# Kernel tuning notes

Measured on AMD Instinct MI355X. Metric: run time of the kernel, lower is better.

Reference implementation:

```python
import jax, jax.numpy as jnp
import numpy as np

B, E, T = 8192, 512, 32


def setup_inputs() -> dict:
    key = jax.random.key(0)
    k1, k2, k3, k4, k5, k6 = jax.random.split(key, 6)
    s1 = 1.0 / np.sqrt(E)  # torch nn.Linear default init scale (uniform bound)
    return {
        "g_exp": jax.random.normal(k1, (B, E), dtype=jnp.float32),
        "tissue_vector": jax.random.randint(k2, (B, 1), 0, T, dtype=jnp.int64),
        # per-tissue head params: Linear(E,E) then Linear(E,1)
        "W1": jax.random.uniform(k3, (T, E, E), jnp.float32, -s1, s1),
        "b1": jax.random.uniform(k4, (T, E), jnp.float32, -s1, s1),
        "W2": jax.random.uniform(k5, (T, E), jnp.float32, -s1, s1),
        "b2": jax.random.uniform(k6, (T,), jnp.float32, -s1, s1),
    }


def reference(g_exp, tissue_vector, W1, b1, W2, b2):
    # Each sample b is routed through the MLP head of its tissue id.
    # Vectorized: run every sample through every tissue head, then select.
    # h[b,t,:] = GELU(g_exp[b] @ W1[t] + b1[t])
    h = jax.nn.gelu(jnp.einsum("be,teh->bth", g_exp, W1) + b1[None, :, :],
                    approximate=False)  # exact erf GELU, matches torch nn.GELU
    # y[b,t] = softplus(h[b,t] @ W2[t] + b2[t])   (Softplus since loss_fn='poisson')
    y = jax.nn.softplus(jnp.einsum("bth,th->bt", h, W2) + b2[None, :])
    tid = tissue_vector[:, 0]  # [B], tissue id per sample
    return jnp.take_along_axis(y, tid[:, None], axis=1)  # [B, 1]
```

## Files before the change

kernel.cpp:

```cpp
#include <hip/hip_runtime.h>
#include <hip/hip_bf16.h>
#include <math.h>

#define B_N 8192
#define E_N 512
#define T_N 32
#define BP 520

typedef short bf16x8 __attribute__((ext_vector_type(8)));
typedef float f32x4 __attribute__((ext_vector_type(4)));

#define WS_OFFS   256
#define WS_RANK   512
#define WS_ORDER  33280
#define WS_YACC   66048
#define WS_YACC8  98816
#define WS_REQ    (WS_YACC8 + 8 * B_N * 4)

typedef __attribute__((address_space(1))) const unsigned int gas_u32;
typedef __attribute__((address_space(3))) unsigned int las_u32;

static __device__ __forceinline__ unsigned short f2bf(float f) {
    unsigned int u = __float_as_uint(f);
    unsigned int r = u + 0x7fffu + ((u >> 16) & 1u);
    return (unsigned short)(r >> 16);
}

static __device__ __forceinline__ unsigned int pk2(float a, float b) {
    __hip_bfloat162 h = __float22bfloat162_rn(float2{a, b});
    unsigned int u;
    __builtin_memcpy(&u, &h, 4);
    return u;
}

__global__ __launch_bounds__(512, 1) void k_gemm_mfma(
    const float* __restrict__ g_exp, const float* __restrict__ W1,
    const int* __restrict__ tv, const float* __restrict__ b1,
    const float* __restrict__ W2, float* __restrict__ yacc8) {
    int wi = blockIdx.x;
    int t = wi & 31, nt = wi >> 5;
    int n0 = nt * 64;

    int tid = threadIdx.x;
    int w = tid >> 6, lane = tid & 63;
    int quad = (lane >> 4) & 3, l15 = lane & 15;

    __shared__ __align__(16) unsigned short Bs[64 * BP];
    __shared__ __align__(16) float As[3][128 * 32];
    __shared__ int rows_s[512];
    __shared__ int wsum[8];

    float b1v[4], w2v[4];
#pragma unroll
    for (int ni = 0; ni < 4; ++ni) {
        int n = t * E_N + n0 + ni * 16 + l15;
        b1v[ni] = b1[n];
        w2v[ni] = W2[n];
    }

    int tvals[16];
    const int4* tvp = (const int4*)(tv + tid * 16);
#pragma unroll
    for (int j = 0; j < 4; ++j) ((int4*)tvals)[j] = tvp[j];
    int myc = 0;
#pragma unroll
    for (int j = 0; j < 16; ++j) myc += (tvals[j] == t) ? 1 : 0;
    int inc = myc;
#pragma unroll
    for (int o = 1; o < 64; o <<= 1) {
        int u = __shfl_up(inc, o, 64);
        if (lane >= o) inc += u;
    }
    if (lane == 63) wsum[w] = inc;
    rows_s[tid] = 0;
    __syncthreads();
    int n_t = 0, wbase = 0;
#pragma unroll
    for (int i = 0; i < 8; ++i) {
        int v = wsum[i];
        n_t += v;
        if (i < w) wbase += v;
    }
    int nt_c = n_t > 512 ? 512 : n_t;
    int rk = wbase + inc - myc;
#pragma unroll
    for (int j = 0; j < 16; ++j)
        if (tvals[j] == t) {
            int rr = rk++;
            if (rr < 512) rows_s[rr] = tid * 16 + j;
        }

    const float* Wsrc = W1 + (size_t)t * E_N * E_N + n0;
    unsigned int* Bw = (unsigned int*)Bs;
#pragma unroll
    for (int i = 0; i < 8; ++i) {
        int flat = i * 512 + tid;
        int k2 = flat >> 4, nq = flat & 15;
        float4 va = *(const float4*)(Wsrc + (size_t)(2 * k2) * E_N + nq * 4);
        float4 vb = *(const float4*)(Wsrc + (size_t)(2 * k2 + 1) * E_N + nq * 4);
        Bw[(nq * 4 + 0) * 260 + k2] = pk2(va.x, vb.x);
        Bw[(nq * 4 + 1) * 260 + k2] = pk2(va.y, vb.y);
        Bw[(nq * 4 + 2) * 260 + k2] = pk2(va.z, vb.z);
        Bw[(nq * 4 + 3) * 260 + k2] = pk2(va.w, vb.w);
    }
    __syncthreads();

    int d0 = tid, d1 = tid + 512;
    int ar0 = d0 >> 3, ac0 = (d0 & 7) ^ (ar0 & 7);
    int ar1 = d1 >> 3, ac1 = (d1 & 7) ^ (ar1 & 7);

    int lrow = w * 16 + l15;
    int c0 = (quad * 2) ^ (lrow & 7);
    int c1 = (quad * 2 + 1) ^ (lrow & 7);

    float* slab = yacc8 + (size_t)nt * B_N;

    int MC = (nt_c + 127) >> 7;
    for (int mc = 0; mc < MC; ++mc) {
        const float* pA0 = g_exp + (size_t)rows_s[mc * 128 + ar0] * E_N + ac0 * 4;
        const float* pA1 = g_exp + (size_t)rows_s[mc * 128 + ar1] * E_N + ac1 * 4;

#define ISSUE(kk) do {                                                                      \
        __builtin_amdgcn_global_load_lds((gas_u32*)(pA0 + (kk) * 32),                       \
                                         (las_u32*)&As[(kk) % 3][d0 * 4], 16, 0, 0);        \
        __builtin_amdgcn_global_load_lds((gas_u32*)(pA1 + (kk) * 32),                       \
                                         (las_u32*)&As[(kk) % 3][d1 * 4], 16, 0, 0);        \
    } while (0)

        ISSUE(0);
        ISSUE(1);

        f32x4 acc[4];
#pragma unroll
        for (int ni = 0; ni < 4; ++ni) acc[ni] = (f32x4){0.f, 0.f, 0.f, 0.f};

#define STAGE(it, W) do {                                                                   \
        asm volatile("s_waitcnt vmcnt(%0)" :: "n"(W) : "memory");                           \
        asm volatile("s_barrier" ::: "memory");                                             \
        const float* Ab = &As[(it) % 3][0];                                                 \
        f32x4 lo = *(const f32x4*)(Ab + (lrow * 8 + c0) * 4);                               \
        f32x4 hi = *(const f32x4*)(Ab + (lrow * 8 + c1) * 4);                               \
        unsigned int uu[4] = {pk2(lo[0], lo[1]), pk2(lo[2], lo[3]),                         \
                              pk2(hi[0], hi[1]), pk2(hi[2], hi[3])};                        \
        bf16x8 af;                                                                          \
        __builtin_memcpy(&af, uu, 16);                                                      \
        _Pragma("unroll") for (int ni = 0; ni < 4; ++ni) {                                  \
            bf16x8 bfr = *(const bf16x8*)(Bs + (ni * 16 + l15) * BP + (it) * 32 + quad * 8);\
            acc[ni] = __builtin_amdgcn_mfma_f32_16x16x32_bf16(af, bfr, acc[ni], 0, 0, 0);   \
        }                                                                                   \
        if ((it) + 2 < 16) ISSUE((it) + 2);                                                 \
    } while (0)

        STAGE(0, 2);  STAGE(1, 2);  STAGE(2, 2);  STAGE(3, 2);
        STAGE(4, 2);  STAGE(5, 2);  STAGE(6, 2);  STAGE(7, 2);
        STAGE(8, 2);  STAGE(9, 2);  STAGE(10, 2); STAGE(11, 2);
        STAGE(12, 2); STAGE(13, 2); STAGE(14, 2); STAGE(15, 0);
#undef STAGE
#undef ISSUE

        float pr[4] = {0.f, 0.f, 0.f, 0.f};
#pragma unroll
        for (int ni = 0; ni < 4; ++ni) {
#pragma unroll
            for (int r = 0; r < 4; ++r) {
                float u = acc[ni][r] + b1v[ni];
                float gg = 0.5f * u * (1.f + erff(u * 0.70710678118654752f));
                pr[r] = fmaf(gg, w2v[ni], pr[r]);
            }
        }
#pragma unroll
        for (int off = 1; off <= 8; off <<= 1)
#pragma unroll
            for (int r = 0; r < 4; ++r) pr[r] += __shfl_xor(pr[r], off, 64);

        if (l15 == 0) {
#pragma unroll
            for (int r = 0; r < 4; ++r) {
                int rr = mc * 128 + w * 16 + quad * 4 + r;
                if (rr < nt_c) slab[rows_s[rr]] = pr[r];
            }
        }
    }
}

__global__ void k_final8(const float* __restrict__ yacc8, const int* __restrict__ tv,
                         const float* __restrict__ b2, float* __restrict__ out) {
    int b = blockIdx.x * blockDim.x + threadIdx.x;
    if (b < B_N) {
        float x = b2[tv[b]];
#pragma unroll
        for (int s = 0; s < 8; ++s) x += yacc8[(size_t)s * B_N + b];
        out[b] = fmaxf(x, 0.f) + log1pf(expf(-fabsf(x)));
    }
}

__global__ __launch_bounds__(256) void k_prep_sb(
    const int* __restrict__ tv, int* __restrict__ offs_g,
    int* __restrict__ rank, int* __restrict__ order, float* __restrict__ yacc) {
    __shared__ int lh[4][32], wcur[4][32], offs_s[33];
    int tid = threadIdx.x, w = tid >> 6;
    if (tid < 128) lh[tid >> 5][tid & 31] = 0;
    __syncthreads();
    int tval[32];
#pragma unroll
    for (int c = 0; c < 32; ++c) tval[c] = tv[c * 256 + tid];
#pragma unroll
    for (int c = 0; c < 32; ++c) atomicAdd(&lh[w][tval[c]], 1);
    __syncthreads();
    if (tid < 32) {
        int s = lh[0][tid] + lh[1][tid] + lh[2][tid] + lh[3][tid];
        int excl = 0;
#pragma unroll
        for (int i = 0; i < 32; ++i) {
            int v = __shfl(s, i, 64);
            if (i < tid) excl += v;
        }
        offs_s[tid] = excl;
        offs_g[tid] = excl;
        if (tid == 31) { offs_s[32] = excl + s; offs_g[32] = excl + s; }
    }
    __syncthreads();
    if (tid < 128) {
        int ww = tid >> 5, t = tid & 31;
        int s = offs_s[t];
        for (int w2 = 0; w2 < ww; ++w2) s += lh[w2][t];
        wcur[ww][t] = s;
    }
    __syncthreads();
#pragma unroll
    for (int c = 0; c < 32; ++c) {
        int b = c * 256 + tid;
        int pos = atomicAdd(&wcur[w][tval[c]], 1);
        rank[b] = pos;
        order[pos] = b;
    }
    float4 z = make_float4(0.f, 0.f, 0.f, 0.f);
#pragma unroll
    for (int c = 0; c < 8; ++c) *(float4*)(yacc + (c * 256 + tid) * 4) = z;
}

__global__ __launch_bounds__(256) void fb_gemm(
    const float* __restrict__ g_exp, const float* __restrict__ W1,
    const float* __restrict__ b1, const float* __restrict__ W2,
    const int* __restrict__ offs, const int* __restrict__ order,
    float* __restrict__ yacc) {
    int t = blockIdx.z;
    int base = offs[t];
    int n_t = offs[t + 1] - base;
    int m0 = blockIdx.y * 64;
    if (m0 >= n_t) return;
    int n0 = blockIdx.x * 128;

    __shared__ float As2[32][68];
    __shared__ float Bs2[32][128];
    __shared__ int sidx[64];

    int tid = threadIdx.x;
    if (tid < 64) {
        int m = m0 + tid;
        sidx[tid] = (m < n_t) ? order[base + m] : -1;
    }
    __syncthreads();

    int ty = tid >> 4, tx = tid & 15;
    float acc[4][8];
#pragma unroll
    for (int r = 0; r < 4; ++r)
#pragma unroll
        for (int c = 0; c < 8; ++c) acc[r][c] = 0.f;

    for (int k0 = 0; k0 < E_N; k0 += 32) {
#pragma unroll
        for (int p = 0; p < 2; ++p) {
            int idx = tid + 256 * p;
            int row = idx >> 3, kcq = idx & 7;
            int s = sidx[row];
            float4 v = make_float4(0.f, 0.f, 0.f, 0.f);
            if (s >= 0) v = *(const float4*)(g_exp + (size_t)s * E_N + k0 + kcq * 4);
            As2[kcq * 4 + 0][row] = v.x;
            As2[kcq * 4 + 1][row] = v.y;
            As2[kcq * 4 + 2][row] = v.z;
            As2[kcq * 4 + 3][row] = v.w;
        }
#pragma unroll
        for (int p = 0; p < 4; ++p) {
            int idx = tid + 256 * p;
            int kr = idx >> 5, c4 = idx & 31;
            *(float4*)(&Bs2[kr][c4 * 4]) =
                *(const float4*)(W1 + ((size_t)t * E_N + (k0 + kr)) * E_N + n0 + c4 * 4);
        }
        __syncthreads();
#pragma unroll
        for (int e = 0; e < 32; ++e) {
            float4 a = *(const float4*)(&As2[e][ty * 4]);
            float4 bA = *(const float4*)(&Bs2[e][tx * 4]);
            float4 bB = *(const float4*)(&Bs2[e][tx * 4 + 64]);
            float av[4] = {a.x, a.y, a.z, a.w};
            float bv[8] = {bA.x, bA.y, bA.z, bA.w, bB.x, bB.y, bB.z, bB.w};
#pragma unroll
            for (int r = 0; r < 4; ++r)
#pragma unroll
                for (int c = 0; c < 8; ++c) acc[r][c] = fmaf(av[r], bv[c], acc[r][c]);
        }
        __syncthreads();
    }

    float pr[4] = {0.f, 0.f, 0.f, 0.f};
#pragma unroll
    for (int c = 0; c < 8; ++c) {
        int n = n0 + tx * 4 + ((c >= 4) ? 64 : 0) + (c & 3);
        float bb = b1[t * E_N + n];
        float w2 = W2[t * E_N + n];
#pragma unroll
        for (int r = 0; r < 4; ++r) {
            float u = acc[r][c] + bb;
            float g = 0.5f * u * (1.f + erff(u * 0.70710678118654752f));
            pr[r] = fmaf(g, w2, pr[r]);
        }
    }
#pragma unroll
    for (int off = 8; off >= 1; off >>= 1)
#pragma unroll
        for (int r = 0; r < 4; ++r) pr[r] += __shfl_xor(pr[r], off, 64);

    if (tx == 0) {
#pragma unroll
        for (int r = 0; r < 4; ++r) {
            int m = m0 + ty * 4 + r;
            if (m < n_t) atomicAdd(&yacc[sidx[ty * 4 + r]], pr[r]);
        }
    }
}

__global__ void fb_final(const float* __restrict__ yacc, const int* __restrict__ tv,
                         const float* __restrict__ b2, float* __restrict__ out) {
    int b = blockIdx.x * blockDim.x + threadIdx.x;
    if (b < B_N) {
        float x = yacc[b] + b2[tv[b]];
        out[b] = fmaxf(x, 0.f) + log1pf(expf(-fabsf(x)));
    }
}

extern "C" void kernel_launch(void* const* d_in, const int* in_sizes, int n_in,
                              void* d_out, int out_size, void* d_ws, size_t ws_size,
                              hipStream_t stream) {
    const float* g_exp = (const float*)d_in[0];
    const int*   tv    = (const int*)d_in[1];
    const float* W1    = (const float*)d_in[2];
    const float* b1    = (const float*)d_in[3];
    const float* W2    = (const float*)d_in[4];
    const float* b2    = (const float*)d_in[5];
    float* out = (float*)d_out;

    char* ws = (char*)d_ws;

    if (ws_size >= (size_t)WS_REQ) {
        float* yacc8 = (float*)(ws + WS_YACC8);
        k_gemm_mfma<<<256, 512, 0, stream>>>(g_exp, W1, tv, b1, W2, yacc8);
        k_final8<<<32, 256, 0, stream>>>(yacc8, tv, b2, out);
    } else {
        int* offs   = (int*)(ws + WS_OFFS);
        int* rank   = (int*)(ws + WS_RANK);
        int* order  = (int*)(ws + WS_ORDER);
        float* yacc = (float*)(ws + WS_YACC);
        k_prep_sb<<<1, 256, 0, stream>>>(tv, offs, rank, order, yacc);
        fb_gemm<<<dim3(4, 8, 32), 256, 0, stream>>>(g_exp, W1, b1, W2, offs, order, yacc);
        fb_final<<<32, 256, 0, stream>>>(yacc, tv, b2, out);
    }
}
```

Measured before the change: 112.0 us.

## Use per-wave A staging buffers without block barriers and flatten the M-chunk pipeline

Each wave now gathers its own 16 rows of g_exp into a private 4-deep LDS ring, so the per-stage s_barrier is dropped and the prefetch distance grows from 2 to 3. The M-chunk and K loops are merged into one flat stage sequence, so prefetch continues across chunk boundaries and the GELU/W2 epilogue runs inline when a chunk finishes. The B tile in LDS also gets an XOR swizzle on the k index to reduce bank conflicts on fragment reads. In exchange, LDS use for A rises and the fully unrolled 16-stage body becomes a runtime loop with index arithmetic in each stage.

```diff
diff --git a/kernel.cpp b/kernel.cpp
--- a/kernel.cpp
+++ b/kernel.cpp
@@ -46,7 +46,7 @@
     int quad = (lane >> 4) & 3, l15 = lane & 15;
 
     __shared__ __align__(16) unsigned short Bs[64 * BP];
-    __shared__ __align__(16) float As[3][128 * 32];
+    __shared__ __align__(16) float As[8][4][512];
     __shared__ int rows_s[512];
     __shared__ int wsum[8];
 
@@ -98,88 +98,90 @@
         int k2 = flat >> 4, nq = flat & 15;
         float4 va = *(const float4*)(Wsrc + (size_t)(2 * k2) * E_N + nq * 4);
         float4 vb = *(const float4*)(Wsrc + (size_t)(2 * k2 + 1) * E_N + nq * 4);
-        Bw[(nq * 4 + 0) * 260 + k2] = pk2(va.x, vb.x);
-        Bw[(nq * 4 + 1) * 260 + k2] = pk2(va.y, vb.y);
-        Bw[(nq * 4 + 2) * 260 + k2] = pk2(va.z, vb.z);
-        Bw[(nq * 4 + 3) * 260 + k2] = pk2(va.w, vb.w);
-    }
-    __syncthreads();
-
-    int d0 = tid, d1 = tid + 512;
-    int ar0 = d0 >> 3, ac0 = (d0 & 7) ^ (ar0 & 7);
-    int ar1 = d1 >> 3, ac1 = (d1 & 7) ^ (ar1 & 7);
-
-    int lrow = w * 16 + l15;
-    int c0 = (quad * 2) ^ (lrow & 7);
-    int c1 = (quad * 2 + 1) ^ (lrow & 7);
-
-    float* slab = yacc8 + (size_t)nt * B_N;
-
-    int MC = (nt_c + 127) >> 7;
-    for (int mc = 0; mc < MC; ++mc) {
-        const float* pA0 = g_exp + (size_t)rows_s[mc * 128 + ar0] * E_N + ac0 * 4;
-        const float* pA1 = g_exp + (size_t)rows_s[mc * 128 + ar1] * E_N + ac1 * 4;
-
-#define ISSUE(kk) do {                                                                      \
-        __builtin_amdgcn_global_load_lds((gas_u32*)(pA0 + (kk) * 32),                       \
-                                         (las_u32*)&As[(kk) % 3][d0 * 4], 16, 0, 0);        \
-        __builtin_amdgcn_global_load_lds((gas_u32*)(pA1 + (kk) * 32),                       \
-                                         (las_u32*)&As[(kk) % 3][d1 * 4], 16, 0, 0);        \
+        int ksw = k2 ^ ((nq & 3) << 2);
+        Bw[(nq * 4 + 0) * 260 + ksw] = pk2(va.x, vb.x);
+        Bw[(nq * 4 + 1) * 260 + ksw] = pk2(va.y, vb.y);
+        Bw[(nq * 4 + 2) * 260 + ksw] = pk2(va.z, vb.z);
+        Bw[(nq * 4 + 3) * 260 + ksw] = pk2(va.w, vb.w);
+    }
+    __syncthreads();
+
+    if (nt_c > 0) {
+        int MC = (nt_c + 127) >> 7;
+        int NT = MC * 16;
+
+        int r0 = lane >> 3, r1 = r0 + 8;
+        int kc = (lane & 7) ^ r0;
+        float* Aw = &As[w][0][0];
+
+        int c0 = (quad * 2) ^ (l15 & 7);
+        int c1 = (quad * 2 + 1) ^ (l15 & 7);
+        int bq = quad ^ ((l15 >> 2) & 3);
+
+        float* slab = yacc8 + (size_t)nt * B_N;
+
+        f32x4 acc[4];
+#pragma unroll
+        for (int ni = 0; ni < 4; ++ni) acc[ni] = (f32x4){0.f, 0.f, 0.f, 0.f};
+
+#define ISSUE(jj) do {                                                                     \
+        int _mc = (jj) >> 4, _kk = (jj) & 15;                                              \
+        int _rb = _mc * 128 + w * 16;                                                      \
+        const float* _s0 = g_exp + (size_t)rows_s[_rb + r0] * E_N + _kk * 32 + kc * 4;     \
+        const float* _s1 = g_exp + (size_t)rows_s[_rb + r1] * E_N + _kk * 32 + kc * 4;     \
+        float* _d = Aw + ((jj) & 3) * 512;                                                 \
+        __builtin_amdgcn_global_load_lds((gas_u32*)_s0, (las_u32*)(_d + lane * 4), 16,0,0);\
+        __builtin_amdgcn_global_load_lds((gas_u32*)_s1, (las_u32*)(_d + (lane+64)*4),      \
+                                         16, 0, 0);                                        \
     } while (0)
 
-        ISSUE(0);
-        ISSUE(1);
-
-        f32x4 acc[4];
-#pragma unroll
-        for (int ni = 0; ni < 4; ++ni) acc[ni] = (f32x4){0.f, 0.f, 0.f, 0.f};
-
-#define STAGE(it, W) do {                                                                   \
-        asm volatile("s_waitcnt vmcnt(%0)" :: "n"(W) : "memory");                           \
-        asm volatile("s_barrier" ::: "memory");                                             \
-        const float* Ab = &As[(it) % 3][0];                                                 \
-        f32x4 lo = *(const f32x4*)(Ab + (lrow * 8 + c0) * 4);                               \
-        f32x4 hi = *(const f32x4*)(Ab + (lrow * 8 + c1) * 4);                               \
-        unsigned int uu[4] = {pk2(lo[0], lo[1]), pk2(lo[2], lo[3]),                         \
-                              pk2(hi[0], hi[1]), pk2(hi[2], hi[3])};                        \
-        bf16x8 af;                                                                          \
-        __builtin_memcpy(&af, uu, 16);                                                      \
-        _Pragma("unroll") for (int ni = 0; ni < 4; ++ni) {                                  \
-            bf16x8 bfr = *(const bf16x8*)(Bs + (ni * 16 + l15) * BP + (it) * 32 + quad * 8);\
-            acc[ni] = __builtin_amdgcn_mfma_f32_16x16x32_bf16(af, bfr, acc[ni], 0, 0, 0);   \
-        }                                                                                   \
-        if ((it) + 2 < 16) ISSUE((it) + 2);                                                 \
+#define EPILOGUE(mcv) do {                                                                 \
+        float pr[4] = {0.f, 0.f, 0.f, 0.f};                                                \
+        _Pragma("unroll") for (int ni = 0; ni < 4; ++ni)                                   \
+            _Pragma("unroll") for (int r = 0; r < 4; ++r) {                                \
+                float u = acc[ni][r] + b1v[ni];                                            \
+                float gg = 0.5f * u * (1.f + erff(u * 0.70710678118654752f));              \
+                pr[r] = fmaf(gg, w2v[ni], pr[r]);                                          \
+            }                                                                              \
+        _Pragma("unroll") for (int off = 1; off <= 8; off <<= 1)                           \
+            _Pragma("unroll") for (int r = 0; r < 4; ++r)                                  \
+                pr[r] += __shfl_xor(pr[r], off, 64);                                       \
+        if (l15 == 0) {                                                                    \
+            _Pragma("unroll") for (int r = 0; r < 4; ++r) {                                \
+                int rr = (mcv) * 128 + w * 16 + quad * 4 + r;                              \
+                if (rr < nt_c) slab[rows_s[rr]] = pr[r];                                   \
+            }                                                                              \
+        }                                                                                  \
+        _Pragma("unroll") for (int ni = 0; ni < 4; ++ni)                                   \
+            acc[ni] = (f32x4){0.f, 0.f, 0.f, 0.f};                                         \
     } while (0)
 
-        STAGE(0, 2);  STAGE(1, 2);  STAGE(2, 2);  STAGE(3, 2);
-        STAGE(4, 2);  STAGE(5, 2);  STAGE(6, 2);  STAGE(7, 2);
-        STAGE(8, 2);  STAGE(9, 2);  STAGE(10, 2); STAGE(11, 2);
-        STAGE(12, 2); STAGE(13, 2); STAGE(14, 2); STAGE(15, 0);
+#define STAGE(jj, W, DOISSUE) do {                                                         \
+        asm volatile("s_waitcnt vmcnt(%0)" :: "n"(W) : "memory");                          \
+        const float* Ab = Aw + ((jj) & 3) * 512;                                           \
+        f32x4 lo = *(const f32x4*)(Ab + l15 * 32 + c0 * 4);                                \
+        f32x4 hi = *(const f32x4*)(Ab + l15 * 32 + c1 * 4);                                \
+        unsigned int uu[4] = {pk2(lo[0], lo[1]), pk2(lo[2], lo[3]),                        \
+                              pk2(hi[0], hi[1]), pk2(hi[2], hi[3])};                       \
+        bf16x8 af;                                                                         \
+        __builtin_memcpy(&af, uu, 16);                                                     \
+        int _it = (jj) & 15;                                                               \
+        _Pragma("unroll") for (int ni = 0; ni < 4; ++ni) {                                 \
+            bf16x8 bfr = *(const bf16x8*)(Bs + (ni * 16 + l15) * BP + _it * 32 + bq * 8);  \
+            acc[ni] = __builtin_amdgcn_mfma_f32_16x16x32_bf16(af, bfr, acc[ni], 0, 0, 0);  \
+        }                                                                                  \
+        if (DOISSUE) ISSUE((jj) + 3);                                                      \
+        if ((_it) == 15) EPILOGUE((jj) >> 4);                                              \
+    } while (0)
+
+        ISSUE(0); ISSUE(1); ISSUE(2);
+        for (int j = 0; j < NT - 3; ++j) STAGE(j, 4, 1);
+        STAGE(NT - 3, 4, 0);
+        STAGE(NT - 2, 2, 0);
+        STAGE(NT - 1, 0, 0);
 #undef STAGE
+#undef EPILOGUE
 #undef ISSUE
-
-        float pr[4] = {0.f, 0.f, 0.f, 0.f};
-#pragma unroll
-        for (int ni = 0; ni < 4; ++ni) {
-#pragma unroll
-            for (int r = 0; r < 4; ++r) {
-                float u = acc[ni][r] + b1v[ni];
-                float gg = 0.5f * u * (1.f + erff(u * 0.70710678118654752f));
-                pr[r] = fmaf(gg, w2v[ni], pr[r]);
-            }
-        }
-#pragma unroll
-        for (int off = 1; off <= 8; off <<= 1)
-#pragma unroll
-            for (int r = 0; r < 4; ++r) pr[r] += __shfl_xor(pr[r], off, 64);
-
-        if (l15 == 0) {
-#pragma unroll
-            for (int r = 0; r < 4; ++r) {
-                int rr = mc * 128 + w * 16 + quad * 4 + r;
-                if (rr < nt_c) slab[rows_s[rr]] = pr[r];
-            }
-        }
     }
 }
 
```

Result: slower. 121.7 us (+8.6%).
